# Kernel tuning notes

Hardware: AMD Instinct MI355X
Metric: run time of the kernel (lower is better)

## Reference

```python
import jax, jax.numpy as jnp
import numpy as np

N = 262144
MUL0, MUL1, MUL2 = 128, 64, 32          # multiplicities of 0e, 1o, 2e
D0, D1, D2 = MUL0, MUL1 * 3, MUL2 * 5   # flat dims: 128, 192, 160
NG = MUL1 + MUL2                        # 96 gate scalars (0e)
NS = MUL0 + NG                          # 224 scalar outputs of the Linear


def _norm2mom_cst(f):
    # e3nn normalize2mom: rescale activation so E_{x~N(0,1)}[f(x)^2] = 1
    xs = np.random.default_rng(0).standard_normal(1_000_000).astype(np.float32)
    return float(1.0 / np.sqrt(np.mean(np.asarray(f(jnp.asarray(xs))) ** 2)))

CST_SILU = _norm2mom_cst(jax.nn.silu)
CST_RELU = _norm2mom_cst(jax.nn.relu)


def setup_inputs() -> dict:
    key = jax.random.key(0)
    k = jax.random.split(key, 5)
    return {
        "x": jax.random.normal(k[0], (N, D0 + D1 + D2), jnp.float32),
        "W0": jax.random.normal(k[1], (MUL0, NS), jnp.float32),
        "b0": jax.random.normal(k[2], (NS,), jnp.float32),
        "W1": jax.random.normal(k[3], (MUL1, MUL1), jnp.float32),
        "W2": jax.random.normal(k[4], (MUL2, MUL2), jnp.float32),
    }


def reference(x, W0, b0, W1, W2):
    n = x.shape[0]
    # split input into irrep blocks: [n,128] 0e, [n,64,3] 1o, [n,32,5] 2e
    x0 = x[:, :D0]
    x1 = x[:, D0:D0 + D1].reshape(n, MUL1, 3)
    x2 = x[:, D0 + D1:].reshape(n, MUL2, 5)
    # e3nn o3.Linear: per-irrep block matmul with 1/sqrt(fan_in) path norm;
    # bias only on scalar (0e) outputs
    s = x0 @ W0 * (1.0 / np.sqrt(MUL0)) + b0                      # [n,224]
    v = jnp.einsum('nim,ij->njm', x1, W1) * (1.0 / np.sqrt(MUL1))  # [n,64,3]
    t = jnp.einsum('nim,ij->njm', x2, W2) * (1.0 / np.sqrt(MUL2))  # [n,32,5]
    # e3nn Gate: silu on the 128 true scalars, relu on the 96 gates,
    # gated irreps multiplied channelwise by their gate scalar
    scalars = CST_SILU * jax.nn.silu(s[:, :MUL0])                  # [n,128]
    gates = CST_RELU * jax.nn.relu(s[:, MUL0:])                    # [n,96]
    gv = (v * gates[:, :MUL1, None]).reshape(n, D1)                # [n,192]
    gt = (t * gates[:, MUL1:, None]).reshape(n, D2)                # [n,160]
    return jnp.concatenate([scalars, gv, gt], axis=-1)            # [n,480]
```

## Files before the change

### kernel.cpp

```cpp
#include <hip/hip_runtime.h>

#define NROWS   262144
#define DIN     480
#define DOUT    480

#define M_TILE  32
#define XSTR    360

#define CST_SILU 1.6765290f
#define CST_RELU 1.4142135623730951f
#define INV_S128 0.08838834764831845f
#define INV_S64  0.125f
#define INV_S32  0.17677669529663687f

#define WS_FRAGS 66
#define WS_BYTES (WS_FRAGS * 64 * 16)

typedef short bf16x8 __attribute__((ext_vector_type(8)));
typedef short s16x4  __attribute__((ext_vector_type(4)));
typedef float f32x4  __attribute__((ext_vector_type(4)));

__device__ __forceinline__ ushort f2bf(float f) {
    unsigned u = __float_as_uint(f);
    u = (u + 0x7FFFu + ((u >> 16) & 1u)) >> 16;
    return (ushort)u;
}

__device__ __forceinline__ bf16x8 load_b_frag(const float* __restrict__ W, int ldw,
                                              int kbase, int nbase, int lane) {
    int n  = nbase + (lane & 15);
    int k0 = kbase + ((lane >> 4) << 3);
    bf16x8 f;
#pragma unroll
    for (int e = 0; e < 8; ++e) f[e] = (short)f2bf(W[(k0 + e) * ldw + n]);
    return f;
}

__global__ __launch_bounds__(64) void prep_frags(
        const float* __restrict__ W0, const float* __restrict__ W1,
        const float* __restrict__ W2, ushort* __restrict__ ws) {
    const int b = blockIdx.x, lane = threadIdx.x;
    const int lr = lane & 15, kg = lane >> 4;
    const float* W; int ldw, n, k0;
    if (b < 56)      { W = W0; ldw = 224; n = (b >> 2) * 16 + lr; k0 = (b & 3) * 32 + (kg << 3); }
    else if (b < 64) { int t = b - 56; W = W1; ldw = 64; n = (t >> 1) * 16 + lr; k0 = (t & 1) * 32 + (kg << 3); }
    else             { W = W2; ldw = 32; n = (b - 64) * 16 + lr; k0 = (kg << 3); }
    bf16x8 f;
#pragma unroll
    for (int e = 0; e < 8; ++e) f[e] = (short)f2bf(W[(k0 + e) * ldw + n]);
    *reinterpret_cast<bf16x8*>(ws + (b * 64 + lane) * 8) = f;
}

template <bool PRE>
__global__ __launch_bounds__(256, 4) void percep_kernel(
        const float* __restrict__ x,  const float* __restrict__ W0,
        const float* __restrict__ bias0, const float* __restrict__ W1,
        const float* __restrict__ W2, float* __restrict__ out,
        const ushort* __restrict__ ws) {
    __shared__ __align__(16) ushort xs[M_TILE * XSTR];

    const int tid  = threadIdx.x;
    const int lane = tid & 63;
    const int wid  = tid >> 6;
    const int lr   = lane & 15;
    const int kg   = lane >> 4;
    const int row0 = blockIdx.x * M_TILE;
    const bf16x8* F = reinterpret_cast<const bf16x8*>(ws);

#pragma unroll
    for (int it = 0; it < 2; ++it) {
        int idx = tid + it * 256;
        int row = idx >> 4, g = idx & 15;
        const float4* p = reinterpret_cast<const float4*>(x + (row0 + row) * DIN + 128 + 12 * g);
        float4 q0 = p[0], q1 = p[1], q2 = p[2];
        float v[12] = { q0.x, q0.y, q0.z, q0.w, q1.x, q1.y, q1.z, q1.w, q2.x, q2.y, q2.z, q2.w };
#pragma unroll
        for (int m = 0; m < 3; ++m) {
            s16x4 o = { (short)f2bf(v[m]), (short)f2bf(v[m + 3]),
                        (short)f2bf(v[m + 6]), (short)f2bf(v[m + 9]) };
            *reinterpret_cast<s16x4*>(&xs[row * XSTR + 64 * m + 4 * g]) = o;
        }
    }
    {
        int row = tid >> 3, g = tid & 7;
        const float4* p = reinterpret_cast<const float4*>(x + (row0 + row) * DIN + 320 + 20 * g);
        float4 q0 = p[0], q1 = p[1], q2 = p[2], q3 = p[3], q4 = p[4];
        float v[20] = { q0.x, q0.y, q0.z, q0.w, q1.x, q1.y, q1.z, q1.w, q2.x, q2.y, q2.z, q2.w,
                        q3.x, q3.y, q3.z, q3.w, q4.x, q4.y, q4.z, q4.w };
#pragma unroll
        for (int m = 0; m < 5; ++m) {
            s16x4 o = { (short)f2bf(v[m]), (short)f2bf(v[m + 5]),
                        (short)f2bf(v[m + 10]), (short)f2bf(v[m + 15]) };
            *reinterpret_cast<s16x4*>(&xs[row * XSTR + 192 + 32 * m + 4 * g]) = o;
        }
    }

    bf16x8 aS[2][4];
#pragma unroll
    for (int rf = 0; rf < 2; ++rf)
#pragma unroll
        for (int kk = 0; kk < 4; ++kk) {
            const float4* p = reinterpret_cast<const float4*>(
                x + (row0 + rf * 16 + lr) * DIN + kk * 32 + (kg << 3));
            float4 u0 = p[0], u1 = p[1];
            bf16x8 a = { (short)f2bf(u0.x), (short)f2bf(u0.y), (short)f2bf(u0.z), (short)f2bf(u0.w),
                         (short)f2bf(u1.x), (short)f2bf(u1.y), (short)f2bf(u1.z), (short)f2bf(u1.w) };
            aS[rf][kk] = a;
        }

    f32x4 gV[2], gT[2];

    auto gate_tile = [&](int st, f32x4* g) {
        bf16x8 b[4];
#pragma unroll
        for (int kk = 0; kk < 4; ++kk)
            b[kk] = PRE ? F[(st * 4 + kk) * 64 + lane]
                        : load_b_frag(W0, 224, kk * 32, st * 16, lane);
        float bias = bias0[st * 16 + lr];
#pragma unroll
        for (int rf = 0; rf < 2; ++rf) {
            f32x4 acc = { 0.f, 0.f, 0.f, 0.f };
#pragma unroll
            for (int kk = 0; kk < 4; ++kk)
                acc = __builtin_amdgcn_mfma_f32_16x16x32_bf16(aS[rf][kk], b[kk], acc, 0, 0, 0);
#pragma unroll
            for (int r = 0; r < 4; ++r) {
                float s = acc[r] * INV_S128 + bias;
                g[rf][r] = fmaxf(s, 0.f) * CST_RELU;
            }
        }
    };
    auto silu_tile = [&](int st) {
        bf16x8 b[4];
#pragma unroll
        for (int kk = 0; kk < 4; ++kk)
            b[kk] = PRE ? F[(st * 4 + kk) * 64 + lane]
                        : load_b_frag(W0, 224, kk * 32, st * 16, lane);
        float bias = bias0[st * 16 + lr];
#pragma unroll
        for (int rf = 0; rf < 2; ++rf) {
            f32x4 acc = { 0.f, 0.f, 0.f, 0.f };
#pragma unroll
            for (int kk = 0; kk < 4; ++kk)
                acc = __builtin_amdgcn_mfma_f32_16x16x32_bf16(aS[rf][kk], b[kk], acc, 0, 0, 0);
#pragma unroll
            for (int r = 0; r < 4; ++r) {
                float s = acc[r] * INV_S128 + bias;
                float val = CST_SILU * s * __builtin_amdgcn_rcpf(1.f + __expf(-s));
                out[(row0 + rf * 16 + (kg << 2) + r) * DOUT + st * 16 + lr] = val;
            }
        }
    };

    if      (wid == 0) { gate_tile(8,  gV); gate_tile(12, gT); silu_tile(0); }
    else if (wid == 1) { gate_tile(9,  gV); gate_tile(13, gT); silu_tile(1); }
    else if (wid == 2) { gate_tile(10, gV); silu_tile(2); silu_tile(3); silu_tile(4); }
    else               { gate_tile(11, gV); silu_tile(5); silu_tile(6); silu_tile(7); }

    __syncthreads();

    {
        const int vu = wid;
        bf16x8 bv0 = PRE ? F[(56 + vu * 2) * 64 + lane]     : load_b_frag(W1, 64, 0,  vu * 16, lane);
        bf16x8 bv1 = PRE ? F[(56 + vu * 2 + 1) * 64 + lane] : load_b_frag(W1, 64, 32, vu * 16, lane);
        const int j = vu * 16 + lr;
#pragma unroll
        for (int rf = 0; rf < 2; ++rf) {
            const ushort* base = &xs[(rf * 16 + lr) * XSTR + (kg << 3)];
            f32x4 a0 = {0,0,0,0}, a1 = {0,0,0,0}, a2 = {0,0,0,0};
            a0 = __builtin_amdgcn_mfma_f32_16x16x32_bf16(*reinterpret_cast<const bf16x8*>(base +   0), bv0, a0, 0, 0, 0);
            a0 = __builtin_amdgcn_mfma_f32_16x16x32_bf16(*reinterpret_cast<const bf16x8*>(base +  32), bv1, a0, 0, 0, 0);
            a1 = __builtin_amdgcn_mfma_f32_16x16x32_bf16(*reinterpret_cast<const bf16x8*>(base +  64), bv0, a1, 0, 0, 0);
            a1 = __builtin_amdgcn_mfma_f32_16x16x32_bf16(*reinterpret_cast<const bf16x8*>(base +  96), bv1, a1, 0, 0, 0);
            a2 = __builtin_amdgcn_mfma_f32_16x16x32_bf16(*reinterpret_cast<const bf16x8*>(base + 128), bv0, a2, 0, 0, 0);
            a2 = __builtin_amdgcn_mfma_f32_16x16x32_bf16(*reinterpret_cast<const bf16x8*>(base + 160), bv1, a2, 0, 0, 0);
#pragma unroll
            for (int r = 0; r < 4; ++r) {
                int row = rf * 16 + (kg << 2) + r;
                float g = gV[rf][r] * INV_S64;
                float* po = out + (row0 + row) * DOUT + 128 + 3 * j;
                po[0] = a0[r] * g; po[1] = a1[r] * g; po[2] = a2[r] * g;
            }
        }
    }

    if (wid < 2) {
        bf16x8 bt = PRE ? F[(64 + wid) * 64 + lane] : load_b_frag(W2, 32, 0, wid * 16, lane);
        const int j = wid * 16 + lr;
#pragma unroll
        for (int rf = 0; rf < 2; ++rf) {
            const ushort* base = &xs[(rf * 16 + lr) * XSTR + 192 + (kg << 3)];
            f32x4 z = {0,0,0,0};
            f32x4 a0 = __builtin_amdgcn_mfma_f32_16x16x32_bf16(*reinterpret_cast<const bf16x8*>(base +   0), bt, z, 0, 0, 0);
            f32x4 a1 = __builtin_amdgcn_mfma_f32_16x16x32_bf16(*reinterpret_cast<const bf16x8*>(base +  32), bt, z, 0, 0, 0);
            f32x4 a2 = __builtin_amdgcn_mfma_f32_16x16x32_bf16(*reinterpret_cast<const bf16x8*>(base +  64), bt, z, 0, 0, 0);
            f32x4 a3 = __builtin_amdgcn_mfma_f32_16x16x32_bf16(*reinterpret_cast<const bf16x8*>(base +  96), bt, z, 0, 0, 0);
            f32x4 a4 = __builtin_amdgcn_mfma_f32_16x16x32_bf16(*reinterpret_cast<const bf16x8*>(base + 128), bt, z, 0, 0, 0);
#pragma unroll
            for (int r = 0; r < 4; ++r) {
                int row = rf * 16 + (kg << 2) + r;
                float g = gT[rf][r] * INV_S32;
                float* po = out + (row0 + row) * DOUT + 320 + 5 * j;
                po[0] = a0[r] * g; po[1] = a1[r] * g; po[2] = a2[r] * g;
                po[3] = a3[r] * g; po[4] = a4[r] * g;
            }
        }
    }
}

extern "C" void kernel_launch(void* const* d_in, const int* in_sizes, int n_in,
                              void* d_out, int out_size, void* d_ws, size_t ws_size,
                              hipStream_t stream) {
    const float* x  = (const float*)d_in[0];
    const float* W0 = (const float*)d_in[1];
    const float* b0 = (const float*)d_in[2];
    const float* W1 = (const float*)d_in[3];
    const float* W2 = (const float*)d_in[4];
    float* out = (float*)d_out;
    dim3 grid(NROWS / M_TILE), block(256);
    if (ws_size >= WS_BYTES) {
        hipLaunchKernelGGL(prep_frags, dim3(WS_FRAGS), dim3(64), 0, stream, W0, W1, W2, (ushort*)d_ws);
        hipLaunchKernelGGL((percep_kernel<true>), grid, block, 0, stream,
                           x, W0, b0, W1, W2, out, (const ushort*)d_ws);
    } else {
        hipLaunchKernelGGL((percep_kernel<false>), grid, block, 0, stream,
                           x, W0, b0, W1, W2, out, (const ushort*)d_ws);
    }
}
```

Measured before the change: 248.8 us.

## Rebalance waves by row-fragment and column half, stage scalars in LDS

Each wave now owns one 16-row fragment and half of the output columns, so all four waves do equal work instead of the old uneven split (two waves had two gate tiles plus one silu tile, the others one gate tile plus three silu tiles). The scalar 0e block is also staged through shared memory with coalesced float4 loads, replacing per-lane strided global reads. The LDS row stride grows to fit it. The sync moves before the scalar matmul. bf16 conversion switches to packed intrinsic conversion. B fragments are reloaded per row fragment rather than reused across two, which adds some weight-load traffic.

```diff
diff --git a/kernel.cpp b/kernel.cpp
--- a/kernel.cpp
+++ b/kernel.cpp
@@ -1,11 +1,12 @@
 #include <hip/hip_runtime.h>
+#include <hip/hip_bf16.h>
 
 #define NROWS   262144
 #define DIN     480
 #define DOUT    480
 
 #define M_TILE  32
-#define XSTR    360
+#define XSTR    488
 
 #define CST_SILU 1.6765290f
 #define CST_RELU 1.4142135623730951f
@@ -17,13 +18,17 @@
 #define WS_BYTES (WS_FRAGS * 64 * 16)
 
 typedef short bf16x8 __attribute__((ext_vector_type(8)));
-typedef short s16x4  __attribute__((ext_vector_type(4)));
 typedef float f32x4  __attribute__((ext_vector_type(4)));
 
 __device__ __forceinline__ ushort f2bf(float f) {
     unsigned u = __float_as_uint(f);
     u = (u + 0x7FFFu + ((u >> 16) & 1u)) >> 16;
     return (ushort)u;
+}
+
+__device__ __forceinline__ unsigned pk2(float a, float b) {
+    __hip_bfloat162 h = __float22bfloat162_rn(float2{a, b});
+    return *reinterpret_cast<unsigned*>(&h);
 }
 
 __device__ __forceinline__ bf16x8 load_b_frag(const float* __restrict__ W, int ldw,
@@ -64,9 +69,19 @@
     const int wid  = tid >> 6;
     const int lr   = lane & 15;
     const int kg   = lane >> 4;
+    const int rf   = wid >> 1;
+    const int half = wid & 1;
     const int row0 = blockIdx.x * M_TILE;
     const bf16x8* F = reinterpret_cast<const bf16x8*>(ws);
 
+#pragma unroll
+    for (int it = 0; it < 4; ++it) {
+        int idx = tid + it * 256;
+        int row = idx >> 5, c4 = idx & 31;
+        const float4 v = reinterpret_cast<const float4*>(x + (row0 + row) * DIN)[c4];
+        uint2 o = { pk2(v.x, v.y), pk2(v.z, v.w) };
+        *reinterpret_cast<uint2*>(&xs[row * XSTR + c4 * 4]) = o;
+    }
 #pragma unroll
     for (int it = 0; it < 2; ++it) {
         int idx = tid + it * 256;
@@ -76,9 +91,8 @@
         float v[12] = { q0.x, q0.y, q0.z, q0.w, q1.x, q1.y, q1.z, q1.w, q2.x, q2.y, q2.z, q2.w };
 #pragma unroll
         for (int m = 0; m < 3; ++m) {
-            s16x4 o = { (short)f2bf(v[m]), (short)f2bf(v[m + 3]),
-                        (short)f2bf(v[m + 6]), (short)f2bf(v[m + 9]) };
-            *reinterpret_cast<s16x4*>(&xs[row * XSTR + 64 * m + 4 * g]) = o;
+            uint2 o = { pk2(v[m], v[m + 3]), pk2(v[m + 6], v[m + 9]) };
+            *reinterpret_cast<uint2*>(&xs[row * XSTR + 128 + 64 * m + 4 * g]) = o;
         }
     }
     {
@@ -89,121 +103,108 @@
                         q3.x, q3.y, q3.z, q3.w, q4.x, q4.y, q4.z, q4.w };
 #pragma unroll
         for (int m = 0; m < 5; ++m) {
-            s16x4 o = { (short)f2bf(v[m]), (short)f2bf(v[m + 5]),
-                        (short)f2bf(v[m + 10]), (short)f2bf(v[m + 15]) };
-            *reinterpret_cast<s16x4*>(&xs[row * XSTR + 192 + 32 * m + 4 * g]) = o;
-        }
-    }
-
-    bf16x8 aS[2][4];
-#pragma unroll
-    for (int rf = 0; rf < 2; ++rf)
+            uint2 o = { pk2(v[m], v[m + 5]), pk2(v[m + 10], v[m + 15]) };
+            *reinterpret_cast<uint2*>(&xs[row * XSTR + 320 + 32 * m + 4 * g]) = o;
+        }
+    }
+    __syncthreads();
+
+    bf16x8 aS[4];
+#pragma unroll
+    for (int kk = 0; kk < 4; ++kk)
+        aS[kk] = *reinterpret_cast<const bf16x8*>(
+            &xs[(rf * 16 + lr) * XSTR + kk * 32 + (kg << 3)]);
+
+    f32x4 gV0, gV1, gT;
+    const int gt0 = half ? 10 : 8, gt1 = half ? 11 : 9, gt2 = half ? 13 : 12;
+
+    auto s_acc = [&](int st) -> f32x4 {
+        f32x4 acc = { 0.f, 0.f, 0.f, 0.f };
 #pragma unroll
         for (int kk = 0; kk < 4; ++kk) {
-            const float4* p = reinterpret_cast<const float4*>(
-                x + (row0 + rf * 16 + lr) * DIN + kk * 32 + (kg << 3));
-            float4 u0 = p[0], u1 = p[1];
-            bf16x8 a = { (short)f2bf(u0.x), (short)f2bf(u0.y), (short)f2bf(u0.z), (short)f2bf(u0.w),
-                         (short)f2bf(u1.x), (short)f2bf(u1.y), (short)f2bf(u1.z), (short)f2bf(u1.w) };
-            aS[rf][kk] = a;
-        }
-
-    f32x4 gV[2], gT[2];
-
-    auto gate_tile = [&](int st, f32x4* g) {
-        bf16x8 b[4];
-#pragma unroll
-        for (int kk = 0; kk < 4; ++kk)
-            b[kk] = PRE ? F[(st * 4 + kk) * 64 + lane]
-                        : load_b_frag(W0, 224, kk * 32, st * 16, lane);
+            bf16x8 b = PRE ? F[(st * 4 + kk) * 64 + lane]
+                           : load_b_frag(W0, 224, kk * 32, st * 16, lane);
+            acc = __builtin_amdgcn_mfma_f32_16x16x32_bf16(aS[kk], b, acc, 0, 0, 0);
+        }
+        return acc;
+    };
+    auto gate_tile = [&](int st) -> f32x4 {
+        f32x4 acc = s_acc(st);
         float bias = bias0[st * 16 + lr];
-#pragma unroll
-        for (int rf = 0; rf < 2; ++rf) {
-            f32x4 acc = { 0.f, 0.f, 0.f, 0.f };
-#pragma unroll
-            for (int kk = 0; kk < 4; ++kk)
-                acc = __builtin_amdgcn_mfma_f32_16x16x32_bf16(aS[rf][kk], b[kk], acc, 0, 0, 0);
-#pragma unroll
-            for (int r = 0; r < 4; ++r) {
-                float s = acc[r] * INV_S128 + bias;
-                g[rf][r] = fmaxf(s, 0.f) * CST_RELU;
+        f32x4 g;
+#pragma unroll
+        for (int r = 0; r < 4; ++r) {
+            float s = acc[r] * INV_S128 + bias;
+            g[r] = fmaxf(s, 0.f) * CST_RELU;
+        }
+        return g;
+    };
+    gV0 = gate_tile(gt0);
+    gV1 = gate_tile(gt1);
+    gT  = gate_tile(gt2);
+#pragma unroll
+    for (int t = 0; t < 4; ++t) {
+        int st = half * 4 + t;
+        f32x4 acc = s_acc(st);
+        float bias = bias0[st * 16 + lr];
+#pragma unroll
+        for (int r = 0; r < 4; ++r) {
+            float s = acc[r] * INV_S128 + bias;
+            float val = CST_SILU * s * __builtin_amdgcn_rcpf(1.f + __expf(-s));
+            out[(row0 + rf * 16 + (kg << 2) + r) * DOUT + st * 16 + lr] = val;
+        }
+    }
+
+    {
+        bf16x8 aV[3][2];
+#pragma unroll
+        for (int m = 0; m < 3; ++m)
+#pragma unroll
+            for (int kk = 0; kk < 2; ++kk)
+                aV[m][kk] = *reinterpret_cast<const bf16x8*>(
+                    &xs[(rf * 16 + lr) * XSTR + 128 + m * 64 + kk * 32 + (kg << 3)]);
+#pragma unroll
+        for (int jt = 0; jt < 2; ++jt) {
+            const int jtg = half * 2 + jt;
+            f32x4 a0 = {0,0,0,0}, a1 = {0,0,0,0}, a2 = {0,0,0,0};
+#pragma unroll
+            for (int kk = 0; kk < 2; ++kk) {
+                bf16x8 b = PRE ? F[(56 + jtg * 2 + kk) * 64 + lane]
+                               : load_b_frag(W1, 64, kk * 32, jtg * 16, lane);
+                a0 = __builtin_amdgcn_mfma_f32_16x16x32_bf16(aV[0][kk], b, a0, 0, 0, 0);
+                a1 = __builtin_amdgcn_mfma_f32_16x16x32_bf16(aV[1][kk], b, a1, 0, 0, 0);
+                a2 = __builtin_amdgcn_mfma_f32_16x16x32_bf16(aV[2][kk], b, a2, 0, 0, 0);
             }
-        }
-    };
-    auto silu_tile = [&](int st) {
-        bf16x8 b[4];
-#pragma unroll
-        for (int kk = 0; kk < 4; ++kk)
-            b[kk] = PRE ? F[(st * 4 + kk) * 64 + lane]
-                        : load_b_frag(W0, 224, kk * 32, st * 16, lane);
-        float bias = bias0[st * 16 + lr];
-#pragma unroll
-        for (int rf = 0; rf < 2; ++rf) {
-            f32x4 acc = { 0.f, 0.f, 0.f, 0.f };
-#pragma unroll
-            for (int kk = 0; kk < 4; ++kk)
-                acc = __builtin_amdgcn_mfma_f32_16x16x32_bf16(aS[rf][kk], b[kk], acc, 0, 0, 0);
-#pragma unroll
-            for (int r = 0; r < 4; ++r) {
-                float s = acc[r] * INV_S128 + bias;
-                float val = CST_SILU * s * __builtin_amdgcn_rcpf(1.f + __expf(-s));
-                out[(row0 + rf * 16 + (kg << 2) + r) * DOUT + st * 16 + lr] = val;
-            }
-        }
-    };
-
-    if      (wid == 0) { gate_tile(8,  gV); gate_tile(12, gT); silu_tile(0); }
-    else if (wid == 1) { gate_tile(9,  gV); gate_tile(13, gT); silu_tile(1); }
-    else if (wid == 2) { gate_tile(10, gV); silu_tile(2); silu_tile(3); silu_tile(4); }
-    else               { gate_tile(11, gV); silu_tile(5); silu_tile(6); silu_tile(7); }
-
-    __syncthreads();
-
-    {
-        const int vu = wid;
-        bf16x8 bv0 = PRE ? F[(56 + vu * 2) * 64 + lane]     : load_b_frag(W1, 64, 0,  vu * 16, lane);
-        bf16x8 bv1 = PRE ? F[(56 + vu * 2 + 1) * 64 + lane] : load_b_frag(W1, 64, 32, vu * 16, lane);
-        const int j = vu * 16 + lr;
-#pragma unroll
-        for (int rf = 0; rf < 2; ++rf) {
-            const ushort* base = &xs[(rf * 16 + lr) * XSTR + (kg << 3)];
-            f32x4 a0 = {0,0,0,0}, a1 = {0,0,0,0}, a2 = {0,0,0,0};
-            a0 = __builtin_amdgcn_mfma_f32_16x16x32_bf16(*reinterpret_cast<const bf16x8*>(base +   0), bv0, a0, 0, 0, 0);
-            a0 = __builtin_amdgcn_mfma_f32_16x16x32_bf16(*reinterpret_cast<const bf16x8*>(base +  32), bv1, a0, 0, 0, 0);
-            a1 = __builtin_amdgcn_mfma_f32_16x16x32_bf16(*reinterpret_cast<const bf16x8*>(base +  64), bv0, a1, 0, 0, 0);
-            a1 = __builtin_amdgcn_mfma_f32_16x16x32_bf16(*reinterpret_cast<const bf16x8*>(base +  96), bv1, a1, 0, 0, 0);
-            a2 = __builtin_amdgcn_mfma_f32_16x16x32_bf16(*reinterpret_cast<const bf16x8*>(base + 128), bv0, a2, 0, 0, 0);
-            a2 = __builtin_amdgcn_mfma_f32_16x16x32_bf16(*reinterpret_cast<const bf16x8*>(base + 160), bv1, a2, 0, 0, 0);
+            const f32x4& gv = jt ? gV1 : gV0;
+            int j = jtg * 16 + lr;
 #pragma unroll
             for (int r = 0; r < 4; ++r) {
                 int row = rf * 16 + (kg << 2) + r;
-                float g = gV[rf][r] * INV_S64;
+                float g = gv[r] * INV_S64;
                 float* po = out + (row0 + row) * DOUT + 128 + 3 * j;
                 po[0] = a0[r] * g; po[1] = a1[r] * g; po[2] = a2[r] * g;
             }
         }
     }
 
-    if (wid < 2) {
-        bf16x8 bt = PRE ? F[(64 + wid) * 64 + lane] : load_b_frag(W2, 32, 0, wid * 16, lane);
-        const int j = wid * 16 + lr;
-#pragma unroll
-        for (int rf = 0; rf < 2; ++rf) {
-            const ushort* base = &xs[(rf * 16 + lr) * XSTR + 192 + (kg << 3)];
-            f32x4 z = {0,0,0,0};
-            f32x4 a0 = __builtin_amdgcn_mfma_f32_16x16x32_bf16(*reinterpret_cast<const bf16x8*>(base +   0), bt, z, 0, 0, 0);
-            f32x4 a1 = __builtin_amdgcn_mfma_f32_16x16x32_bf16(*reinterpret_cast<const bf16x8*>(base +  32), bt, z, 0, 0, 0);
-            f32x4 a2 = __builtin_amdgcn_mfma_f32_16x16x32_bf16(*reinterpret_cast<const bf16x8*>(base +  64), bt, z, 0, 0, 0);
-            f32x4 a3 = __builtin_amdgcn_mfma_f32_16x16x32_bf16(*reinterpret_cast<const bf16x8*>(base +  96), bt, z, 0, 0, 0);
-            f32x4 a4 = __builtin_amdgcn_mfma_f32_16x16x32_bf16(*reinterpret_cast<const bf16x8*>(base + 128), bt, z, 0, 0, 0);
-#pragma unroll
-            for (int r = 0; r < 4; ++r) {
-                int row = rf * 16 + (kg << 2) + r;
-                float g = gT[rf][r] * INV_S32;
-                float* po = out + (row0 + row) * DOUT + 320 + 5 * j;
-                po[0] = a0[r] * g; po[1] = a1[r] * g; po[2] = a2[r] * g;
-                po[3] = a3[r] * g; po[4] = a4[r] * g;
-            }
+    {
+        bf16x8 bt = PRE ? F[(64 + half) * 64 + lane]
+                        : load_b_frag(W2, 32, 0, half * 16, lane);
+        const ushort* base = &xs[(rf * 16 + lr) * XSTR + 320 + (kg << 3)];
+        f32x4 z = {0,0,0,0};
+        f32x4 a0 = __builtin_amdgcn_mfma_f32_16x16x32_bf16(*reinterpret_cast<const bf16x8*>(base +   0), bt, z, 0, 0, 0);
+        f32x4 a1 = __builtin_amdgcn_mfma_f32_16x16x32_bf16(*reinterpret_cast<const bf16x8*>(base +  32), bt, z, 0, 0, 0);
+        f32x4 a2 = __builtin_amdgcn_mfma_f32_16x16x32_bf16(*reinterpret_cast<const bf16x8*>(base +  64), bt, z, 0, 0, 0);
+        f32x4 a3 = __builtin_amdgcn_mfma_f32_16x16x32_bf16(*reinterpret_cast<const bf16x8*>(base +  96), bt, z, 0, 0, 0);
+        f32x4 a4 = __builtin_amdgcn_mfma_f32_16x16x32_bf16(*reinterpret_cast<const bf16x8*>(base + 128), bt, z, 0, 0, 0);
+        int j = half * 16 + lr;
+#pragma unroll
+        for (int r = 0; r < 4; ++r) {
+            int row = rf * 16 + (kg << 2) + r;
+            float g = gT[r] * INV_S32;
+            float* po = out + (row0 + row) * DOUT + 320 + 5 * j;
+            po[0] = a0[r] * g; po[1] = a1[r] * g; po[2] = a2[r] * g;
+            po[3] = a3[r] * g; po[4] = a4[r] * g;
         }
     }
 }
```

Result: faster. 222.2 us (-10.7%).
